# Optimization experiments

Measured on AMD Instinct MI355X. Metric: run time of the kernel, lower is better.

The kernel has to match this reference:

```python
import jax, jax.numpy as jnp
import numpy as np
import math

B, S, D = 4, 2048, 512
H, DK, DV = 8, 12, 32

def setup_inputs() -> dict:
    key = jax.random.key(0)
    ks = jax.random.split(key, 12)
    s = 0.02
    return {
        "query": jax.random.normal(ks[0], (B, S, D), jnp.float32),
        "key": jax.random.normal(ks[1], (B, S, D), jnp.float32),
        "value": jax.random.normal(ks[2], (B, S, D), jnp.float32),
        "mask": jax.random.randint(ks[3], (B, 1, S), 0, 2, jnp.int32),
        "Wq": jax.random.normal(ks[4], (D, H * DK), jnp.float32) * s,
        "bq": jnp.zeros((H * DK,), jnp.float32),
        "Wk": jax.random.normal(ks[5], (D, H * DK), jnp.float32) * s,
        "bk": jnp.zeros((H * DK,), jnp.float32),
        "Wv": jax.random.normal(ks[6], (D, H * DV), jnp.float32) * s,
        "bv": jnp.zeros((H * DV,), jnp.float32),
        "Wx": jax.random.normal(ks[7], (H * DV, D), jnp.float32) * s,
        "bx": jnp.zeros((D,), jnp.float32),
    }

def reference(query, key, value, mask, Wq, bq, Wk, bk, Wv, bv, Wx, bx):
    # mask: (B,1,S) -> (B,1,1,S) after unsqueeze(1)
    m = mask[:, None, :, :]  # (B,1,1,S)
    nb = query.shape[0]
    # projections, split heads: (B, S, H*dk) -> (B, H, S, dk)
    q = (query @ Wq + bq).reshape(nb, -1, H, DK).transpose(0, 2, 1, 3)
    k = (key @ Wk + bk).reshape(nb, -1, H, DK).transpose(0, 2, 1, 3)
    v = (value @ Wv + bv).reshape(nb, -1, H, DV).transpose(0, 2, 1, 3)
    scores = jnp.einsum("bhqd,bhkd->bhqk", q, k) / math.sqrt(DK)
    scores = jnp.where(m == 0, jnp.float32(-1e9), scores)
    p_attn = jax.nn.softmax(scores, axis=-1)
    # dropout is identity in eval mode
    x = jnp.einsum("bhqk,bhkd->bhqd", p_attn, v)  # (B,H,S,dv)
    x = x.transpose(0, 2, 1, 3).reshape(nb, -1, H * DV)
    x = x @ Wx + bx
    return (x, p_attn)
```

## Files before the change

### kernel.cpp

```cpp
#include <hip/hip_runtime.h>

#define S_LEN 2048
#define NB 4
#define NH 8

typedef short bfrag8 __attribute__((ext_vector_type(8)));
typedef float f32x16 __attribute__((ext_vector_type(16)));
typedef float f32x4 __attribute__((ext_vector_type(4)));

__device__ __forceinline__ unsigned short f2bf(float x) {
  union { float f; unsigned u; } v; v.f = x;
  unsigned r = v.u + 0x7FFFu + ((v.u >> 16) & 1u);
  return (unsigned short)(r >> 16);
}

__global__ __launch_bounds__(256) void cast_qkv(
    const float* __restrict__ q, const float* __restrict__ k,
    const float* __restrict__ v, unsigned short* __restrict__ dst)
{
  const size_t i4 = (size_t)blockIdx.x * 256 + threadIdx.x;
  const size_t per = (size_t)8192 * 512 / 4;
  const float* src = (i4 < per) ? q : (i4 < 2 * per ? k : v);
  const size_t off = (i4 % per) * 4;
  const float4 vv = *reinterpret_cast<const float4*>(src + off);
  ushort4 o;
  o.x = f2bf(vv.x); o.y = f2bf(vv.y); o.z = f2bf(vv.z); o.w = f2bf(vv.w);
  *reinterpret_cast<ushort4*>(dst + i4 * 4) = o;
}

__global__ __launch_bounds__(256) void transpose_w(
    const float* __restrict__ Wq, const float* __restrict__ Wk,
    const float* __restrict__ Wv, const float* __restrict__ Wx,
    unsigned short* __restrict__ wqT, unsigned short* __restrict__ wkT,
    unsigned short* __restrict__ wvT, unsigned short* __restrict__ wxT)
{
  int i = blockIdx.x * 256 + threadIdx.x;
  if (i < 49152) {
    const int n = i / 512, kk = i % 512;
    wqT[i] = f2bf(Wq[(size_t)kk * 96 + n]);
  } else if (i < 98304) {
    i -= 49152; const int n = i / 512, kk = i % 512;
    wkT[i] = f2bf(Wk[(size_t)kk * 96 + n]);
  } else if (i < 229376) {
    i -= 98304; const int n = i / 512, kk = i % 512;
    wvT[i] = f2bf(Wv[(size_t)kk * 256 + n]);
  } else if (i < 360448) {
    i -= 229376; const int n = i / 256, kk = i % 256;
    wxT[i] = f2bf(Wx[(size_t)kk * 512 + n]);
  }
}

template <int MODE>
__global__ __launch_bounds__(256) void gemm_mfma(
    const unsigned short* __restrict__ A, const unsigned short* __restrict__ BT,
    const float* __restrict__ bias, float* __restrict__ Cf,
    unsigned short* __restrict__ Cb, int M, int N, int K, float oscale)
{
  const int t = threadIdx.x, w = t >> 6, lane = t & 63;
  const int lo = lane & 31, hi = lane >> 5;
  const int r0 = blockIdx.x * 128 + 32 * w;
  const int c0 = blockIdx.y * 32;

  const unsigned short* ap = A + (size_t)(r0 + lo) * K + hi * 8;
  const unsigned short* bp = BT + (size_t)(c0 + lo) * K + hi * 8;

  f32x16 acc;
#pragma unroll
  for (int r = 0; r < 16; ++r) acc[r] = 0.f;

  for (int k0 = 0; k0 < K; k0 += 16) {
    const bfrag8 af = *reinterpret_cast<const bfrag8*>(ap + k0);
    const bfrag8 bf = *reinterpret_cast<const bfrag8*>(bp + k0);
    if constexpr (MODE == 2)
      acc = __builtin_amdgcn_mfma_f32_32x32x16_bf16(bf, af, acc, 0, 0, 0);
    else
      acc = __builtin_amdgcn_mfma_f32_32x32x16_bf16(af, bf, acc, 0, 0, 0);
  }

  if constexpr (MODE == 0) {
    const int c = c0 + lo;
    const float bc = bias[c];
#pragma unroll
    for (int r = 0; r < 16; ++r) {
      const int grow = r0 + (r & 3) + 8 * (r >> 2) + 4 * hi;
      Cf[(size_t)grow * N + c] = acc[r] + bc;
    }
  } else if constexpr (MODE == 1) {
    const int c = c0 + lo;
    const int off = (c / 12) * 16 + (c % 12);
    const float bc = bias[c];
#pragma unroll
    for (int r = 0; r < 16; ++r) {
      const int grow = r0 + (r & 3) + 8 * (r >> 2) + 4 * hi;
      Cb[(size_t)grow * 128 + off] = f2bf((acc[r] + bc) * oscale);
    }
  } else {
    const int s = r0 + lo;
    const int bb = s >> 11, sl = s & (S_LEN - 1);
#pragma unroll
    for (int r = 0; r < 16; ++r) {
      const int c = c0 + (r & 3) + 8 * (r >> 2) + 4 * hi;
      Cb[((size_t)(bb * N + c)) * S_LEN + sl] = f2bf(acc[r] + bias[c]);
    }
  }
}

__global__ __launch_bounds__(256) void fill_pads(
    const int* __restrict__ mask,
    unsigned short* __restrict__ q_bf, unsigned short* __restrict__ k_bf)
{
  const int i = blockIdx.x * 256 + threadIdx.x;
  const int h = i & 7;
  const int s = (i >> 3) & (S_LEN - 1);
  const int b = i >> 14;
  const size_t base = (size_t)(b * S_LEN + s) * 128 + h * 16 + 12;
  ushort4 qp; qp.x = 0x3F80; qp.y = 0; qp.z = 0; qp.w = 0;
  ushort4 kp; kp.x = (mask[b * S_LEN + s] != 0) ? (unsigned short)0
                                                : (unsigned short)0xCE6E;
  kp.y = 0; kp.z = 0; kp.w = 0;
  *reinterpret_cast<ushort4*>(q_bf + base) = qp;
  *reinterpret_cast<ushort4*>(k_bf + base) = kp;
}

__global__ __launch_bounds__(256) void attn_mfma(
    const unsigned short* __restrict__ q_bf,
    const unsigned short* __restrict__ k_bf,
    const unsigned short* __restrict__ vT_bf,
    float* __restrict__ p_out, unsigned short* __restrict__ x_bf)
{
  const int id = blockIdx.x + blockIdx.y * 64;
  const int xcd = id & 7, jj = id >> 3;
  const int bh = 4 * xcd + (jj >> 6);
  const int q0 = (jj & 63) * 32;
  const int b = bh >> 3, h = bh & 7;
  const int t = threadIdx.x, w = t >> 6, lane = t & 63;
  const int lo = lane & 31, hi = lane >> 5;

  __shared__ float red_lds[4][32];
  __shared__ __align__(16) char smbuf[4 * 64 * 20 * 4];
  float (*p_lds)[32][36] = reinterpret_cast<float (*)[32][36]>(smbuf);
  float (*xr)[64][20]    = reinterpret_cast<float (*)[64][20]>(smbuf);

  const bfrag8 qf = *reinterpret_cast<const bfrag8*>(
      q_bf + (size_t)(b * S_LEN + q0 + lo) * 128 + h * 16 + hi * 8);
  const unsigned short* kbase = k_bf + (size_t)b * S_LEN * 128 + h * 16 + hi * 8;

  f32x16 zc;
#pragma unroll
  for (int r = 0; r < 16; ++r) zc[r] = 0.f;

  float sum = 0.f;
  for (int ch = w * 64; ch < S_LEN; ch += 256) {
#pragma unroll
    for (int T = 0; T < 2; ++T) {
      const bfrag8 kf = *reinterpret_cast<const bfrag8*>(
          kbase + (size_t)(ch + T * 32 + lo) * 128);
      const f32x16 sc = __builtin_amdgcn_mfma_f32_32x32x16_bf16(kf, qf, zc, 0, 0, 0);
#pragma unroll
      for (int r = 0; r < 16; ++r) sum += __expf(sc[r]);
    }
  }
  sum += __shfl_xor(sum, 32);
  if (hi == 0) red_lds[w][lo] = sum;
  __syncthreads();
  const float inv = 1.0f /
      (red_lds[0][lo] + red_lds[1][lo] + red_lds[2][lo] + red_lds[3][lo]);

  f32x16 xacc;
#pragma unroll
  for (int r = 0; r < 16; ++r) xacc[r] = 0.f;

  const unsigned short* vbase = vT_bf + (size_t)(b * 256 + h * 32 + lo) * S_LEN;
  float* pg0 = p_out + (size_t)bh * S_LEN * S_LEN + (size_t)q0 * S_LEN;

  for (int ch = w * 64; ch < S_LEN; ch += 256) {
#pragma unroll
    for (int T = 0; T < 2; ++T) {
      const bfrag8 kf = *reinterpret_cast<const bfrag8*>(
          kbase + (size_t)(ch + T * 32 + lo) * 128);
      const f32x16 sc = __builtin_amdgcn_mfma_f32_32x32x16_bf16(kf, qf, zc, 0, 0, 0);

#pragma unroll
      for (int qd = 0; qd < 4; ++qd) {
        f32x4 ev;
        ev.x = __expf(sc[qd * 4 + 0]) * inv;
        ev.y = __expf(sc[qd * 4 + 1]) * inv;
        ev.z = __expf(sc[qd * 4 + 2]) * inv;
        ev.w = __expf(sc[qd * 4 + 3]) * inv;
        *reinterpret_cast<f32x4*>(&p_lds[w][lo][qd * 8 + hi * 4]) = ev;
      }

      float* pg = pg0 + ch + T * 32;
#pragma unroll
      for (int i = 0; i < 4; ++i) {
        const int row = i * 8 + (lane >> 3);
        const int k4  = (lane & 7) * 4;
        const f32x4 pv = *reinterpret_cast<const f32x4*>(&p_lds[w][row][k4]);
        __builtin_nontemporal_store(pv,
            reinterpret_cast<f32x4*>(pg + (size_t)row * S_LEN + k4));
      }

#pragma unroll
      for (int m = 0; m < 2; ++m) {
        const f32x4 pa = *reinterpret_cast<const f32x4*>(&p_lds[w][lo][m * 16 + hi * 8]);
        const f32x4 pb = *reinterpret_cast<const f32x4*>(&p_lds[w][lo][m * 16 + hi * 8 + 4]);
        bfrag8 af;
        af[0] = (short)f2bf(pa.x); af[1] = (short)f2bf(pa.y);
        af[2] = (short)f2bf(pa.z); af[3] = (short)f2bf(pa.w);
        af[4] = (short)f2bf(pb.x); af[5] = (short)f2bf(pb.y);
        af[6] = (short)f2bf(pb.z); af[7] = (short)f2bf(pb.w);
        const bfrag8 vf = *reinterpret_cast<const bfrag8*>(
            vbase + ch + T * 32 + m * 16 + hi * 8);
        xacc = __builtin_amdgcn_mfma_f32_32x32x16_bf16(af, vf, xacc, 0, 0, 0);
      }
    }
  }

  __syncthreads();
#pragma unroll
  for (int r = 0; r < 16; r += 4) {
    f32x4 v4; v4.x = xacc[r]; v4.y = xacc[r + 1]; v4.z = xacc[r + 2]; v4.w = xacc[r + 3];
    *reinterpret_cast<f32x4*>(&xr[w][lane][r]) = v4;
  }
  __syncthreads();
  unsigned short* xw = x_bf + (size_t)(b * S_LEN + q0) * 256 + h * 32 + lo;
#pragma unroll
  for (int j = 0; j < 4; ++j) {
    const int rr = w * 4 + j;
    const float xs = xr[0][lane][rr] + xr[1][lane][rr]
                   + xr[2][lane][rr] + xr[3][lane][rr];
    const int row = j + 8 * w + 4 * hi;
    xw[(size_t)row * 256] = f2bf(xs);
  }
}

extern "C" void kernel_launch(void* const* d_in, const int* in_sizes, int n_in,
                              void* d_out, int out_size, void* d_ws, size_t ws_size,
                              hipStream_t stream) {
  const float* query = (const float*)d_in[0];
  const float* key_  = (const float*)d_in[1];
  const float* value = (const float*)d_in[2];
  const int*   mask  = (const int*)d_in[3];
  const float* Wq = (const float*)d_in[4];
  const float* bq = (const float*)d_in[5];
  const float* Wk = (const float*)d_in[6];
  const float* bk = (const float*)d_in[7];
  const float* Wv = (const float*)d_in[8];
  const float* bv = (const float*)d_in[9];
  const float* Wx = (const float*)d_in[10];
  const float* bx = (const float*)d_in[11];

  const int M = NB * S_LEN;
  float* out_x = (float*)d_out;
  float* out_p = out_x + (size_t)M * 512;

  unsigned short* qkv_bf = (unsigned short*)d_ws;
  unsigned short* wqT = qkv_bf + (size_t)3 * M * 512;
  unsigned short* wkT = wqT + 49152;
  unsigned short* wvT = wkT + 49152;
  unsigned short* wxT = wvT + 131072;
  unsigned short* q_bf = wxT + 131072;
  unsigned short* k_bf = q_bf + (size_t)M * 128;
  unsigned short* vT_bf = k_bf + (size_t)M * 128;
  unsigned short* x_bf = vT_bf + (size_t)NB * 256 * S_LEN;

  const float qscale = 0.28867513459481287f;

  cast_qkv<<<3 * M * 512 / 4 / 256, 256, 0, stream>>>(query, key_, value, qkv_bf);
  transpose_w<<<1408, 256, 0, stream>>>(Wq, Wk, Wv, Wx, wqT, wkT, wvT, wxT);

  const unsigned short* qb = qkv_bf;
  const unsigned short* kb = qkv_bf + (size_t)M * 512;
  const unsigned short* vb = qkv_bf + (size_t)2 * M * 512;

  gemm_mfma<1><<<dim3(M / 128, 3), 256, 0, stream>>>(
      qb, wqT, bq, nullptr, q_bf, M, 96, 512, qscale);
  gemm_mfma<1><<<dim3(M / 128, 3), 256, 0, stream>>>(
      kb, wkT, bk, nullptr, k_bf, M, 96, 512, 1.0f);
  gemm_mfma<2><<<dim3(M / 128, 8), 256, 0, stream>>>(
      vb, wvT, bv, nullptr, vT_bf, M, 256, 512, 1.0f);
  fill_pads<<<NB * S_LEN * NH / 256, 256, 0, stream>>>(mask, q_bf, k_bf);

  attn_mfma<<<dim3(S_LEN / 32, NB * NH), 256, 0, stream>>>(
      q_bf, k_bf, vT_bf, out_p, x_bf);

  gemm_mfma<0><<<dim3(M / 128, 16), 256, 0, stream>>>(
      x_bf, wxT, bx, out_x, nullptr, M, 512, 256, 1.0f);
}
```

Baseline: 190.6 us.

## Fuse input cast, QKV projections and pad fill into one kernel

Removes the separate fp32-to-bf16 cast pass over query/key/value. The projection kernel now reads fp32 directly and converts in registers. Q, K and V projections plus the mask pad fill are merged into one launch with XCD-aware block mapping. V and output projections compute four 32-column tiles per wave, reusing the A fragment. This cuts launches and about 48MB of intermediate traffic, at the cost of more registers and uncoalesced fp32 loads in the projection.

```diff
diff --git a/kernel.cpp b/kernel.cpp
--- a/kernel.cpp
+++ b/kernel.cpp
@@ -12,20 +12,6 @@
   union { float f; unsigned u; } v; v.f = x;
   unsigned r = v.u + 0x7FFFu + ((v.u >> 16) & 1u);
   return (unsigned short)(r >> 16);
-}
-
-__global__ __launch_bounds__(256) void cast_qkv(
-    const float* __restrict__ q, const float* __restrict__ k,
-    const float* __restrict__ v, unsigned short* __restrict__ dst)
-{
-  const size_t i4 = (size_t)blockIdx.x * 256 + threadIdx.x;
-  const size_t per = (size_t)8192 * 512 / 4;
-  const float* src = (i4 < per) ? q : (i4 < 2 * per ? k : v);
-  const size_t off = (i4 % per) * 4;
-  const float4 vv = *reinterpret_cast<const float4*>(src + off);
-  ushort4 o;
-  o.x = f2bf(vv.x); o.y = f2bf(vv.y); o.z = f2bf(vv.z); o.w = f2bf(vv.w);
-  *reinterpret_cast<ushort4*>(dst + i4 * 4) = o;
 }
 
 __global__ __launch_bounds__(256) void transpose_w(
@@ -50,76 +36,111 @@
   }
 }
 
-template <int MODE>
-__global__ __launch_bounds__(256) void gemm_mfma(
-    const unsigned short* __restrict__ A, const unsigned short* __restrict__ BT,
-    const float* __restrict__ bias, float* __restrict__ Cf,
-    unsigned short* __restrict__ Cb, int M, int N, int K, float oscale)
+__global__ __launch_bounds__(256) void proj_qkv(
+    const float* __restrict__ query, const float* __restrict__ key_,
+    const float* __restrict__ value, const int* __restrict__ mask,
+    const unsigned short* __restrict__ wqT, const unsigned short* __restrict__ wkT,
+    const unsigned short* __restrict__ wvT,
+    const float* __restrict__ bq, const float* __restrict__ bk,
+    const float* __restrict__ bv,
+    unsigned short* __restrict__ q_bf, unsigned short* __restrict__ k_bf,
+    unsigned short* __restrict__ vT_bf, float qscale)
 {
+  const int id = blockIdx.x;
+  const int xcd = id & 7, j = id >> 3;
+  const int bxl = j & 7, ys = j >> 3;
+  const int bx = xcd * 8 + bxl;
   const int t = threadIdx.x, w = t >> 6, lane = t & 63;
   const int lo = lane & 31, hi = lane >> 5;
-  const int r0 = blockIdx.x * 128 + 32 * w;
-  const int c0 = blockIdx.y * 32;
-
-  const unsigned short* ap = A + (size_t)(r0 + lo) * K + hi * 8;
-  const unsigned short* bp = BT + (size_t)(c0 + lo) * K + hi * 8;
-
-  f32x16 acc;
-#pragma unroll
-  for (int r = 0; r < 16; ++r) acc[r] = 0.f;
-
-  for (int k0 = 0; k0 < K; k0 += 16) {
-    const bfrag8 af = *reinterpret_cast<const bfrag8*>(ap + k0);
-    const bfrag8 bf = *reinterpret_cast<const bfrag8*>(bp + k0);
-    if constexpr (MODE == 2)
-      acc = __builtin_amdgcn_mfma_f32_32x32x16_bf16(bf, af, acc, 0, 0, 0);
-    else
+  const int r0 = bx * 128 + 32 * w;
+
+  if (ys < 6) {
+    const bool isq = (ys < 3);
+    const float* A = isq ? query : key_;
+    const unsigned short* BT = isq ? wqT : wkT;
+    const float* bias = isq ? bq : bk;
+    unsigned short* Cb = isq ? q_bf : k_bf;
+    const float osc = isq ? qscale : 1.0f;
+    const int c0 = (isq ? ys : ys - 3) * 32;
+
+    const float* ap = A + (size_t)(r0 + lo) * 512 + hi * 8;
+    const unsigned short* bp = BT + (size_t)(c0 + lo) * 512 + hi * 8;
+
+    f32x16 acc;
+#pragma unroll
+    for (int r = 0; r < 16; ++r) acc[r] = 0.f;
+
+    for (int k0 = 0; k0 < 512; k0 += 16) {
+      const float4 a0 = *reinterpret_cast<const float4*>(ap + k0);
+      const float4 a1 = *reinterpret_cast<const float4*>(ap + k0 + 4);
+      bfrag8 af;
+      af[0] = (short)f2bf(a0.x); af[1] = (short)f2bf(a0.y);
+      af[2] = (short)f2bf(a0.z); af[3] = (short)f2bf(a0.w);
+      af[4] = (short)f2bf(a1.x); af[5] = (short)f2bf(a1.y);
+      af[6] = (short)f2bf(a1.z); af[7] = (short)f2bf(a1.w);
+      const bfrag8 bf = *reinterpret_cast<const bfrag8*>(bp + k0);
       acc = __builtin_amdgcn_mfma_f32_32x32x16_bf16(af, bf, acc, 0, 0, 0);
-  }
-
-  if constexpr (MODE == 0) {
-    const int c = c0 + lo;
-    const float bc = bias[c];
-#pragma unroll
-    for (int r = 0; r < 16; ++r) {
-      const int grow = r0 + (r & 3) + 8 * (r >> 2) + 4 * hi;
-      Cf[(size_t)grow * N + c] = acc[r] + bc;
-    }
-  } else if constexpr (MODE == 1) {
+    }
+
     const int c = c0 + lo;
     const int off = (c / 12) * 16 + (c % 12);
     const float bc = bias[c];
 #pragma unroll
     for (int r = 0; r < 16; ++r) {
       const int grow = r0 + (r & 3) + 8 * (r >> 2) + 4 * hi;
-      Cb[(size_t)grow * 128 + off] = f2bf((acc[r] + bc) * oscale);
+      Cb[(size_t)grow * 128 + off] = f2bf((acc[r] + bc) * osc);
+    }
+    if ((c % 12) == 0) {
+      const int hh = c / 12;
+#pragma unroll
+      for (int r = 0; r < 16; ++r) {
+        const int grow = r0 + (r & 3) + 8 * (r >> 2) + 4 * hi;
+        ushort4 pv;
+        pv.x = isq ? (unsigned short)0x3F80
+                   : ((mask[grow] != 0) ? (unsigned short)0
+                                        : (unsigned short)0xCE6E);
+        pv.y = 0; pv.z = 0; pv.w = 0;
+        *reinterpret_cast<ushort4*>(Cb + (size_t)grow * 128 + hh * 16 + 12) = pv;
+      }
     }
   } else {
+    const int ct0 = (ys - 6) * 128;
+    const float* ap = value + (size_t)(r0 + lo) * 512 + hi * 8;
+    const unsigned short* bp = wvT + (size_t)(ct0 + lo) * 512 + hi * 8;
+
+    f32x16 acc[4];
+#pragma unroll
+    for (int tt = 0; tt < 4; ++tt)
+#pragma unroll
+      for (int r = 0; r < 16; ++r) acc[tt][r] = 0.f;
+
+    for (int k0 = 0; k0 < 512; k0 += 16) {
+      const float4 a0 = *reinterpret_cast<const float4*>(ap + k0);
+      const float4 a1 = *reinterpret_cast<const float4*>(ap + k0 + 4);
+      bfrag8 af;
+      af[0] = (short)f2bf(a0.x); af[1] = (short)f2bf(a0.y);
+      af[2] = (short)f2bf(a0.z); af[3] = (short)f2bf(a0.w);
+      af[4] = (short)f2bf(a1.x); af[5] = (short)f2bf(a1.y);
+      af[6] = (short)f2bf(a1.z); af[7] = (short)f2bf(a1.w);
+#pragma unroll
+      for (int tt = 0; tt < 4; ++tt) {
+        const bfrag8 bf = *reinterpret_cast<const bfrag8*>(
+            bp + (size_t)tt * 32 * 512 + k0);
+        acc[tt] = __builtin_amdgcn_mfma_f32_32x32x16_bf16(bf, af, acc[tt], 0, 0, 0);
+      }
+    }
+
     const int s = r0 + lo;
     const int bb = s >> 11, sl = s & (S_LEN - 1);
 #pragma unroll
-    for (int r = 0; r < 16; ++r) {
-      const int c = c0 + (r & 3) + 8 * (r >> 2) + 4 * hi;
-      Cb[((size_t)(bb * N + c)) * S_LEN + sl] = f2bf(acc[r] + bias[c]);
-    }
-  }
-}
-
-__global__ __launch_bounds__(256) void fill_pads(
-    const int* __restrict__ mask,
-    unsigned short* __restrict__ q_bf, unsigned short* __restrict__ k_bf)
-{
-  const int i = blockIdx.x * 256 + threadIdx.x;
-  const int h = i & 7;
-  const int s = (i >> 3) & (S_LEN - 1);
-  const int b = i >> 14;
-  const size_t base = (size_t)(b * S_LEN + s) * 128 + h * 16 + 12;
-  ushort4 qp; qp.x = 0x3F80; qp.y = 0; qp.z = 0; qp.w = 0;
-  ushort4 kp; kp.x = (mask[b * S_LEN + s] != 0) ? (unsigned short)0
-                                                : (unsigned short)0xCE6E;
-  kp.y = 0; kp.z = 0; kp.w = 0;
-  *reinterpret_cast<ushort4*>(q_bf + base) = qp;
-  *reinterpret_cast<ushort4*>(k_bf + base) = kp;
+    for (int tt = 0; tt < 4; ++tt) {
+#pragma unroll
+      for (int r = 0; r < 16; ++r) {
+        const int c = ct0 + tt * 32 + (r & 3) + 8 * (r >> 2) + 4 * hi;
+        vT_bf[((size_t)(bb * 256 + c)) * S_LEN + sl] = f2bf(acc[tt][r] + bv[c]);
+      }
+    }
+  }
 }
 
 __global__ __launch_bounds__(256) void attn_mfma(
@@ -231,6 +252,51 @@
                    + xr[2][lane][rr] + xr[3][lane][rr];
     const int row = j + 8 * w + 4 * hi;
     xw[(size_t)row * 256] = f2bf(xs);
+  }
+}
+
+__global__ __launch_bounds__(256) void out_proj(
+    const unsigned short* __restrict__ x_bf,
+    const unsigned short* __restrict__ wxT,
+    const float* __restrict__ bx, float* __restrict__ out)
+{
+  const int id = blockIdx.x;
+  const int xcd = id & 7, j = id >> 3;
+  const int bxl = j & 7, by = j >> 3;
+  const int bx_ = xcd * 8 + bxl;
+  const int t = threadIdx.x, w = t >> 6, lane = t & 63;
+  const int lo = lane & 31, hi = lane >> 5;
+  const int r0 = bx_ * 128 + 32 * w;
+  const int c00 = by * 128;
+
+  const unsigned short* ap = x_bf + (size_t)(r0 + lo) * 256 + hi * 8;
+  const unsigned short* bp = wxT + (size_t)(c00 + lo) * 256 + hi * 8;
+
+  f32x16 acc[4];
+#pragma unroll
+  for (int tt = 0; tt < 4; ++tt)
+#pragma unroll
+    for (int r = 0; r < 16; ++r) acc[tt][r] = 0.f;
+
+  for (int k0 = 0; k0 < 256; k0 += 16) {
+    const bfrag8 af = *reinterpret_cast<const bfrag8*>(ap + k0);
+#pragma unroll
+    for (int tt = 0; tt < 4; ++tt) {
+      const bfrag8 bf = *reinterpret_cast<const bfrag8*>(
+          bp + (size_t)tt * 32 * 256 + k0);
+      acc[tt] = __builtin_amdgcn_mfma_f32_32x32x16_bf16(af, bf, acc[tt], 0, 0, 0);
+    }
+  }
+
+#pragma unroll
+  for (int tt = 0; tt < 4; ++tt) {
+    const int c = c00 + tt * 32 + lo;
+    const float bc = bx[c];
+#pragma unroll
+    for (int r = 0; r < 16; ++r) {
+      const int grow = r0 + (r & 3) + 8 * (r >> 2) + 4 * hi;
+      out[(size_t)grow * 512 + c] = acc[tt][r] + bc;
+    }
   }
 }
 
@@ -254,11 +320,10 @@
   float* out_x = (float*)d_out;
   float* out_p = out_x + (size_t)M * 512;
 
-  unsigned short* qkv_bf = (unsigned short*)d_ws;
-  unsigned short* wqT = qkv_bf + (size_t)3 * M * 512;
-  unsigned short* wkT = wqT + 49152;
-  unsigned short* wvT = wkT + 49152;
-  unsigned short* wxT = wvT + 131072;
+  unsigned short* wqT  = (unsigned short*)d_ws;
+  unsigned short* wkT  = wqT + 49152;
+  unsigned short* wvT  = wkT + 49152;
+  unsigned short* wxT  = wvT + 131072;
   unsigned short* q_bf = wxT + 131072;
   unsigned short* k_bf = q_bf + (size_t)M * 128;
   unsigned short* vT_bf = k_bf + (size_t)M * 128;
@@ -266,24 +331,14 @@
 
   const float qscale = 0.28867513459481287f;
 
-  cast_qkv<<<3 * M * 512 / 4 / 256, 256, 0, stream>>>(query, key_, value, qkv_bf);
   transpose_w<<<1408, 256, 0, stream>>>(Wq, Wk, Wv, Wx, wqT, wkT, wvT, wxT);
 
-  const unsigned short* qb = qkv_bf;
-  const unsigned short* kb = qkv_bf + (size_t)M * 512;
-  const unsigned short* vb = qkv_bf + (size_t)2 * M * 512;
-
-  gemm_mfma<1><<<dim3(M / 128, 3), 256, 0, stream>>>(
-      qb, wqT, bq, nullptr, q_bf, M, 96, 512, qscale);
-  gemm_mfma<1><<<dim3(M / 128, 3), 256, 0, stream>>>(
-      kb, wkT, bk, nullptr, k_bf, M, 96, 512, 1.0f);
-  gemm_mfma<2><<<dim3(M / 128, 8), 256, 0, stream>>>(
-      vb, wvT, bv, nullptr, vT_bf, M, 256, 512, 1.0f);
-  fill_pads<<<NB * S_LEN * NH / 256, 256, 0, stream>>>(mask, q_bf, k_bf);
+  proj_qkv<<<512, 256, 0, stream>>>(
+      query, key_, value, mask, wqT, wkT, wvT, bq, bk, bv,
+      q_bf, k_bf, vT_bf, qscale);
 
   attn_mfma<<<dim3(S_LEN / 32, NB * NH), 256, 0, stream>>>(
       q_bf, k_bf, vT_bf, out_p, x_bf);
 
-  gemm_mfma<0><<<dim3(M / 128, 16), 256, 0, stream>>>(
-      x_bf, wxT, bx, out_x, nullptr, M, 512, 256, 1.0f);
-}
+  out_proj<<<256, 256, 0, stream>>>(x_bf, wxT, bx, out_x);
+}
```

New measurement: 170.3 us. 10.7% less time.
